# Performance work log

Hardware: AMD Instinct MI355X
Metric: run time of the kernel (lower is better)

## Reference

```python
import jax, jax.numpy as jnp
import numpy as np

NEG = -9e15
ALPHA = 0.2  # leaky relu slope

def setup_inputs() -> dict:
    key = jax.random.key(0)
    k1, k2, k3, k4 = jax.random.split(key, 4)
    N, Fin, Fout = 8192, 512, 256
    h = jax.random.normal(k1, (N, Fin), dtype=jnp.float32)
    adj = jax.random.randint(k2, (N, N), 0, 2, dtype=jnp.int32)
    # xavier_uniform with gain=1.414
    gain = 1.414
    limW = gain * np.sqrt(6.0 / (Fin + Fout))
    W = jax.random.uniform(k3, (Fin, Fout), dtype=jnp.float32, minval=-limW, maxval=limW)
    lima = gain * np.sqrt(6.0 / (2 * Fout + 1))
    a = jax.random.uniform(k4, (2 * Fout, 1), dtype=jnp.float32, minval=-lima, maxval=lima)
    return {"h": h, "adj": adj, "W": W, "a": a}

def reference(h, adj, W, a):
    Fout = W.shape[1]
    Wh = h @ W                                   # [N, Fout]
    # decompose a = [a1; a2]: e_ij = leaky(a1.Wh_i + a2.Wh_j)
    f1 = Wh @ a[:Fout]                           # [N, 1]
    f2 = Wh @ a[Fout:]                           # [N, 1]
    e = jax.nn.leaky_relu(f1 + f2.T, negative_slope=ALPHA)  # [N, N]
    e = jnp.where(adj > 0, e, jnp.float32(NEG))
    attention = jax.nn.softmax(e, axis=1)
    # dropout is identity at inference (training=False)
    h_prime = attention @ Wh                     # [N, Fout]
    return jax.nn.elu(h_prime)
```

## Files before the change

kernel.cpp:

```cpp
#include <hip/hip_runtime.h>
#include <cstdint>
#include <cstddef>

#define ALPHA 0.2f

typedef __attribute__((ext_vector_type(8)))  short short8;
typedef __attribute__((ext_vector_type(16))) float f32x16;

static __device__ __forceinline__ unsigned short f2bf(float x) {
  union { float f; unsigned u; } c; c.f = x;
  unsigned u = c.u;
  unsigned r = (u + 0x7FFFu + ((u >> 16) & 1u)) >> 16;
  return (unsigned short)r;
}
static __device__ __forceinline__ float bf2f(unsigned short b) {
  union { unsigned u; float f; } c; c.u = ((unsigned)b) << 16;
  return c.f;
}

__global__ __launch_bounds__(256, 2) void gemm1(const float* __restrict__ h,
                                                const float* __restrict__ W,
                                                float* __restrict__ Wh) {
  __shared__ float As[32][132];
  __shared__ float Bs[32][64];
  const int t = threadIdx.x;
  const int bid = blockIdx.x;
  const int nb = bid & 3, mb = bid >> 2;
  const int m0 = mb * 128, n0 = nb * 64;
  const int ty = t >> 4, tx = t & 15;
  float acc[8][4];
#pragma unroll
  for (int i = 0; i < 8; i++)
#pragma unroll
    for (int j = 0; j < 4; j++) acc[i][j] = 0.f;

  for (int k0 = 0; k0 < 512; k0 += 32) {
#pragma unroll
    for (int c = 0; c < 4; c++) {
      int m = c * 32 + (t >> 3);
      int kq = (t & 7) * 4;
      float4 v = *(const float4*)&h[(size_t)(m0 + m) * 512 + k0 + kq];
      As[kq + 0][m] = v.x; As[kq + 1][m] = v.y;
      As[kq + 2][m] = v.z; As[kq + 3][m] = v.w;
    }
#pragma unroll
    for (int c = 0; c < 2; c++) {
      int k = c * 16 + (t >> 4);
      int n = (t & 15) * 4;
      *(float4*)&Bs[k][n] = *(const float4*)&W[(size_t)(k0 + k) * 256 + n0 + n];
    }
    __syncthreads();
#pragma unroll
    for (int k = 0; k < 32; k++) {
      float4 a0 = *(float4*)&As[k][ty * 8];
      float4 a1 = *(float4*)&As[k][ty * 8 + 4];
      float4 b  = *(float4*)&Bs[k][tx * 4];
      float av[8] = {a0.x, a0.y, a0.z, a0.w, a1.x, a1.y, a1.z, a1.w};
      float bv[4] = {b.x, b.y, b.z, b.w};
#pragma unroll
      for (int i = 0; i < 8; i++)
#pragma unroll
        for (int j = 0; j < 4; j++) acc[i][j] = fmaf(av[i], bv[j], acc[i][j]);
    }
    __syncthreads();
  }
#pragma unroll
  for (int i = 0; i < 8; i++) {
    float4 v = {acc[i][0], acc[i][1], acc[i][2], acc[i][3]};
    *(float4*)&Wh[(size_t)(m0 + ty * 8 + i) * 256 + n0 + tx * 4] = v;
  }
}

__global__ __launch_bounds__(256) void rowstats(const float* __restrict__ Wh,
                                                const float* __restrict__ a,
                                                float* __restrict__ f1,
                                                float* __restrict__ f2,
                                                unsigned* __restrict__ uvpack,
                                                unsigned short* __restrict__ WhT) {
  const int t = threadIdx.x;
  const int w = t >> 6, lane = t & 63;
  const int i = blockIdx.x * 4 + w;
  float4 wv = *(const float4*)&Wh[(size_t)i * 256 + lane * 4];
  float4 a1 = *(const float4*)&a[lane * 4];
  float4 a2 = *(const float4*)&a[256 + lane * 4];
  float s1 = wv.x * a1.x + wv.y * a1.y + wv.z * a1.z + wv.w * a1.w;
  float s2 = wv.x * a2.x + wv.y * a2.y + wv.z * a2.z + wv.w * a2.w;
#pragma unroll
  for (int off = 32; off; off >>= 1) { s1 += __shfl_xor(s1, off); s2 += __shfl_xor(s2, off); }
  const float wvv[4] = {wv.x, wv.y, wv.z, wv.w};
#pragma unroll
  for (int c = 0; c < 4; c++)
    WhT[(size_t)(lane * 4 + c) * 8192 + i] = f2bf(wvv[c]);
  if (lane == 0) {
    f1[i] = s1; f2[i] = s2;
    float u = __expf(s2), v = __expf(ALPHA * s2);
    uvpack[i] = (unsigned)f2bf(u) | ((unsigned)f2bf(v) << 16);
  }
}

__global__ __launch_bounds__(256) void f2max_k(const float* __restrict__ f2,
                                               float* __restrict__ f2maxp) {
  __shared__ float red[256];
  const int t = threadIdx.x;
  float m = -1e30f;
  for (int c = 0; c < 32; c++) m = fmaxf(m, f2[c * 256 + t]);
  red[t] = m;
  __syncthreads();
  for (int s = 128; s; s >>= 1) {
    if (t < s) red[t] = fmaxf(red[t], red[t + s]);
    __syncthreads();
  }
  if (t == 0) f2maxp[0] = red[0];
}

__global__ __launch_bounds__(256, 2) void attn_main(const int* __restrict__ adj,
                                                    const float* __restrict__ f1,
                                                    const unsigned* __restrict__ uvpack,
                                                    const unsigned short* __restrict__ WhT,
                                                    const float* __restrict__ f2maxp,
                                                    float* __restrict__ accP,
                                                    float* __restrict__ lP) {
  __shared__ unsigned uvs[4096];
  __shared__ __align__(16) unsigned short Pt[32][40];
  __shared__ float lred[32][8];
  const int t = threadIdx.x;
  const int bid = blockIdx.x;
  const int jh = bid & 1;
  const int rb = bid >> 1;
  const int r0 = rb * 32;
  const int jbase = jh * 4096;

#pragma unroll
  for (int c = 0; c < 4; c++) {
    int idx = c * 1024 + t * 4;
    *(uint4*)&uvs[idx] = *(const uint4*)&uvpack[jbase + idx];
  }

  const int r = t >> 3, q = t & 7;
  const float F2max = f2maxp[0];
  const float f1v = f1[r0 + r];
  const float x = f1v + F2max;
  const float M = x > 0.f ? x : ALPHA * x;
  const float Ai = __expf(f1v - M);
  const float Bi = __expf(ALPHA * f1v - M);
  const float Ui = __expf(-f1v);

  const int lane = t & 63, wave = t >> 6;
  const int am = lane & 31, asel = lane >> 5;
  f32x16 acc0 = {}; f32x16 acc1 = {};
  float lpriv = 0.f;

  const int* adjp = adj + (size_t)(r0 + r) * 8192 + jbase + q * 4;
  const unsigned short* bp0 = WhT + (size_t)(wave * 64 + am) * 8192 + jbase + asel * 8;
  const unsigned short* bp1 = bp0 + (size_t)32 * 8192;

  __syncthreads();

  int4 av = *(const int4*)adjp; adjp += 32;
  for (int s = 0; s < 128; s++) {
    int4 avn;
    if (s < 127) { avn = *(const int4*)adjp; }
    adjp += 32;
    uint4 uvq = *(const uint4*)&uvs[s * 32 + q * 4];
    const unsigned uv[4] = {uvq.x, uvq.y, uvq.z, uvq.w};
    const int ad[4] = {av.x, av.y, av.z, av.w};
    float wgt[4];
#pragma unroll
    for (int jj = 0; jj < 4; jj++) {
      float u = bf2f((unsigned short)(uv[jj] & 0xFFFFu));
      float v = bf2f((unsigned short)(uv[jj] >> 16));
      float wv = (u > Ui) ? Ai * u : Bi * v;
      wv = (ad[jj] > 0) ? wv : 0.f;
      wgt[jj] = wv;
    }
    lpriv += (wgt[0] + wgt[1]) + (wgt[2] + wgt[3]);
    unsigned p0 = (unsigned)f2bf(wgt[0]) | ((unsigned)f2bf(wgt[1]) << 16);
    unsigned p1 = (unsigned)f2bf(wgt[2]) | ((unsigned)f2bf(wgt[3]) << 16);
    uint2 pw; pw.x = p0; pw.y = p1;
    *(uint2*)&Pt[r][q * 4] = pw;
    __syncthreads();
#pragma unroll
    for (int hh = 0; hh < 2; hh++) {
      short8 afrag = *(const short8*)&Pt[am][hh * 16 + asel * 8];
      short8 bf0 = *(const short8*)(bp0 + (size_t)s * 32 + hh * 16);
      short8 bf1 = *(const short8*)(bp1 + (size_t)s * 32 + hh * 16);
      acc0 = __builtin_amdgcn_mfma_f32_32x32x16_bf16(afrag, bf0, acc0, 0, 0, 0);
      acc1 = __builtin_amdgcn_mfma_f32_32x32x16_bf16(afrag, bf1, acc1, 0, 0, 0);
    }
    __syncthreads();
    av = avn;
  }

  const size_t base = (size_t)jh * (8192 * 256);
#pragma unroll
  for (int reg = 0; reg < 16; reg++) {
    int rowl = (reg & 3) + 8 * (reg >> 2) + 4 * asel;
    int col = wave * 64 + am;
    accP[base + (size_t)(r0 + rowl) * 256 + col] = acc0[reg];
    accP[base + (size_t)(r0 + rowl) * 256 + col + 32] = acc1[reg];
  }
  lred[r][q] = lpriv;
  __syncthreads();
  if (q == 0) {
    float ssum = 0.f;
#pragma unroll
    for (int k = 0; k < 8; k++) ssum += lred[r][k];
    lP[jh * 8192 + r0 + r] = ssum;
  }
}

__global__ __launch_bounds__(256) void combine(const float* __restrict__ accP,
                                               const float* __restrict__ lP,
                                               float* __restrict__ out) {
  const int idx = (blockIdx.x * 256 + threadIdx.x) * 4;
  const int row = idx >> 8;
  float4 a0 = *(const float4*)&accP[idx];
  float4 a1 = *(const float4*)&accP[(size_t)8192 * 256 + idx];
  float l = lP[row] + lP[8192 + row];
  float inv = 1.0f / fmaxf(l, 1e-30f);
  float vv[4] = {(a0.x + a1.x) * inv, (a0.y + a1.y) * inv,
                 (a0.z + a1.z) * inv, (a0.w + a1.w) * inv};
  float4 o;
  o.x = vv[0] > 0.f ? vv[0] : __expf(vv[0]) - 1.f;
  o.y = vv[1] > 0.f ? vv[1] : __expf(vv[1]) - 1.f;
  o.z = vv[2] > 0.f ? vv[2] : __expf(vv[2]) - 1.f;
  o.w = vv[3] > 0.f ? vv[3] : __expf(vv[3]) - 1.f;
  *(float4*)&out[idx] = o;
}

extern "C" void kernel_launch(void* const* d_in, const int* in_sizes, int n_in,
                              void* d_out, int out_size, void* d_ws, size_t ws_size,
                              hipStream_t stream) {
  const float* h  = (const float*)d_in[0];
  const int* adj  = (const int*)d_in[1];
  const float* W  = (const float*)d_in[2];
  const float* a  = (const float*)d_in[3];
  float* out = (float*)d_out;
  char* ws = (char*)d_ws;

  float* Wh            = (float*)ws;
  float* accP          = (float*)ws;
  unsigned short* WhT  = (unsigned short*)(ws + (size_t)(16u << 20));
  float* f1            = (float*)(ws + (size_t)(20u << 20));
  float* f2            = (float*)(ws + (size_t)(20u << 20) + (32u << 10));
  unsigned* uvpack     = (unsigned*)(ws + (size_t)(20u << 20) + (64u << 10));
  float* f2maxp        = (float*)(ws + (size_t)(20u << 20) + (96u << 10));
  float* lP            = (float*)(ws + (size_t)(20u << 20) + (97u << 10));

  gemm1<<<256, 256, 0, stream>>>(h, W, Wh);
  rowstats<<<2048, 256, 0, stream>>>(Wh, a, f1, f2, uvpack, WhT);
  f2max_k<<<1, 256, 0, stream>>>(f2, f2maxp);
  attn_main<<<512, 256, 0, stream>>>(adj, f1, uvpack, WhT, f2maxp, accP, lP);
  combine<<<2048, 256, 0, stream>>>(accP, lP, out);
}
```

Before: 568.1 us.

## Split-K gemm1, tiled transpose, atomic f2 max, batched double-buffered attention with more splits

The first GEMM is split along K into two partial outputs that later kernels sum, which doubles the block count. The scattered bf16 transpose moves into a separate LDS-tiled kernel, and the single-block f2 max reduction becomes an atomicMax on an order-preserving key. The attention kernel processes four 32-column steps per barrier with a double-buffered, XOR-swizzled P tile and higher occupancy. It uses 4 column splits when the workspace allows, at the cost of extra partial-accumulator traffic in combine.

```diff
diff --git a/kernel.cpp b/kernel.cpp
--- a/kernel.cpp
+++ b/kernel.cpp
@@ -10,8 +10,7 @@
 static __device__ __forceinline__ unsigned short f2bf(float x) {
   union { float f; unsigned u; } c; c.f = x;
   unsigned u = c.u;
-  unsigned r = (u + 0x7FFFu + ((u >> 16) & 1u)) >> 16;
-  return (unsigned short)r;
+  return (unsigned short)((u + 0x7FFFu + ((u >> 16) & 1u)) >> 16);
 }
 static __device__ __forceinline__ float bf2f(unsigned short b) {
   union { unsigned u; float f; } c; c.u = ((unsigned)b) << 16;
@@ -20,13 +19,13 @@
 
 __global__ __launch_bounds__(256, 2) void gemm1(const float* __restrict__ h,
                                                 const float* __restrict__ W,
-                                                float* __restrict__ Wh) {
+                                                float* __restrict__ Whp) {
   __shared__ float As[32][132];
   __shared__ float Bs[32][64];
   const int t = threadIdx.x;
   const int bid = blockIdx.x;
-  const int nb = bid & 3, mb = bid >> 2;
-  const int m0 = mb * 128, n0 = nb * 64;
+  const int nb = bid & 3, kb = (bid >> 2) & 1, mb = bid >> 3;
+  const int m0 = mb * 128, n0 = nb * 64, kbase = kb * 256;
   const int ty = t >> 4, tx = t & 15;
   float acc[8][4];
 #pragma unroll
@@ -34,7 +33,7 @@
 #pragma unroll
     for (int j = 0; j < 4; j++) acc[i][j] = 0.f;
 
-  for (int k0 = 0; k0 < 512; k0 += 32) {
+  for (int k0 = kbase; k0 < kbase + 256; k0 += 32) {
 #pragma unroll
     for (int c = 0; c < 4; c++) {
       int m = c * 32 + (t >> 3);
@@ -64,81 +63,98 @@
     }
     __syncthreads();
   }
+  float* dst = Whp + (size_t)kb * (8192 * 256);
 #pragma unroll
   for (int i = 0; i < 8; i++) {
     float4 v = {acc[i][0], acc[i][1], acc[i][2], acc[i][3]};
-    *(float4*)&Wh[(size_t)(m0 + ty * 8 + i) * 256 + n0 + tx * 4] = v;
-  }
-}
-
-__global__ __launch_bounds__(256) void rowstats(const float* __restrict__ Wh,
+    *(float4*)&dst[(size_t)(m0 + ty * 8 + i) * 256 + n0 + tx * 4] = v;
+  }
+}
+
+__global__ __launch_bounds__(256) void rowstats(const float* __restrict__ Whp,
                                                 const float* __restrict__ a,
                                                 float* __restrict__ f1,
-                                                float* __restrict__ f2,
                                                 unsigned* __restrict__ uvpack,
-                                                unsigned short* __restrict__ WhT) {
+                                                unsigned* __restrict__ f2key) {
   const int t = threadIdx.x;
   const int w = t >> 6, lane = t & 63;
   const int i = blockIdx.x * 4 + w;
-  float4 wv = *(const float4*)&Wh[(size_t)i * 256 + lane * 4];
+  const size_t off = (size_t)i * 256 + lane * 4;
+  float4 v0 = *(const float4*)&Whp[off];
+  float4 v1 = *(const float4*)&Whp[(size_t)8192 * 256 + off];
+  float4 wv = {v0.x + v1.x, v0.y + v1.y, v0.z + v1.z, v0.w + v1.w};
   float4 a1 = *(const float4*)&a[lane * 4];
   float4 a2 = *(const float4*)&a[256 + lane * 4];
   float s1 = wv.x * a1.x + wv.y * a1.y + wv.z * a1.z + wv.w * a1.w;
   float s2 = wv.x * a2.x + wv.y * a2.y + wv.z * a2.z + wv.w * a2.w;
 #pragma unroll
-  for (int off = 32; off; off >>= 1) { s1 += __shfl_xor(s1, off); s2 += __shfl_xor(s2, off); }
-  const float wvv[4] = {wv.x, wv.y, wv.z, wv.w};
-#pragma unroll
-  for (int c = 0; c < 4; c++)
-    WhT[(size_t)(lane * 4 + c) * 8192 + i] = f2bf(wvv[c]);
+  for (int o = 32; o; o >>= 1) { s1 += __shfl_xor(s1, o); s2 += __shfl_xor(s2, o); }
   if (lane == 0) {
-    f1[i] = s1; f2[i] = s2;
+    f1[i] = s1;
     float u = __expf(s2), v = __expf(ALPHA * s2);
     uvpack[i] = (unsigned)f2bf(u) | ((unsigned)f2bf(v) << 16);
-  }
-}
-
-__global__ __launch_bounds__(256) void f2max_k(const float* __restrict__ f2,
-                                               float* __restrict__ f2maxp) {
-  __shared__ float red[256];
-  const int t = threadIdx.x;
-  float m = -1e30f;
-  for (int c = 0; c < 32; c++) m = fmaxf(m, f2[c * 256 + t]);
-  red[t] = m;
+    unsigned ub = __float_as_uint(s2);
+    unsigned key = (ub & 0x80000000u) ? ~ub : (ub | 0x80000000u);
+    atomicMax(f2key, key);
+  }
+}
+
+__global__ __launch_bounds__(256) void transpose_k(const float* __restrict__ Whp,
+                                                   unsigned short* __restrict__ WhT) {
+  __shared__ unsigned short tile[64][264];
+  const int t = threadIdx.x;
+  const int i0 = (blockIdx.x >> 2) * 256, c0 = (blockIdx.x & 3) * 64;
+#pragma unroll
+  for (int it = 0; it < 16; it++) {
+    int i = it * 16 + (t >> 4);
+    int cq = (t & 15) * 4;
+    size_t off = (size_t)(i0 + i) * 256 + c0 + cq;
+    float4 v0 = *(const float4*)&Whp[off];
+    float4 v1 = *(const float4*)&Whp[(size_t)8192 * 256 + off];
+    tile[cq + 0][i] = f2bf(v0.x + v1.x);
+    tile[cq + 1][i] = f2bf(v0.y + v1.y);
+    tile[cq + 2][i] = f2bf(v0.z + v1.z);
+    tile[cq + 3][i] = f2bf(v0.w + v1.w);
+  }
   __syncthreads();
-  for (int s = 128; s; s >>= 1) {
-    if (t < s) red[t] = fmaxf(red[t], red[t + s]);
-    __syncthreads();
-  }
-  if (t == 0) f2maxp[0] = red[0];
-}
-
-__global__ __launch_bounds__(256, 2) void attn_main(const int* __restrict__ adj,
-                                                    const float* __restrict__ f1,
-                                                    const unsigned* __restrict__ uvpack,
-                                                    const unsigned short* __restrict__ WhT,
-                                                    const float* __restrict__ f2maxp,
-                                                    float* __restrict__ accP,
-                                                    float* __restrict__ lP) {
-  __shared__ unsigned uvs[4096];
-  __shared__ __align__(16) unsigned short Pt[32][40];
+  const int c = t >> 2, seg = t & 3;
+#pragma unroll
+  for (int k = 0; k < 8; k++) {
+    int io = (k * 4 + seg) * 8;
+    *(uint4*)&WhT[(size_t)(c0 + c) * 8192 + i0 + io] = *(const uint4*)&tile[c][io];
+  }
+}
+
+template <int JW>
+__global__ __launch_bounds__(256, 4) void attn_main(const int* __restrict__ adj,
+    const float* __restrict__ f1p, const unsigned* __restrict__ uvpack,
+    const unsigned short* __restrict__ WhT, const unsigned* __restrict__ f2key,
+    float* __restrict__ accP, float* __restrict__ lP) {
+  constexpr int JS = 8192 / JW;
+  constexpr int NSTEP = JW / 32;
+  constexpr int KSTEP = 4;
+  constexpr int G = NSTEP / KSTEP;
+  __shared__ unsigned uvs[JW];
+  __shared__ unsigned short Pt[2][32][KSTEP * 32];
   __shared__ float lred[32][8];
   const int t = threadIdx.x;
   const int bid = blockIdx.x;
-  const int jh = bid & 1;
-  const int rb = bid >> 1;
+  const int js = bid & (JS - 1);
+  const int rb = bid / JS;
   const int r0 = rb * 32;
-  const int jbase = jh * 4096;
-
-#pragma unroll
-  for (int c = 0; c < 4; c++) {
+  const int jbase = js * JW;
+
+#pragma unroll
+  for (int c = 0; c < JW / 1024; c++) {
     int idx = c * 1024 + t * 4;
     *(uint4*)&uvs[idx] = *(const uint4*)&uvpack[jbase + idx];
   }
 
   const int r = t >> 3, q = t & 7;
-  const float F2max = f2maxp[0];
-  const float f1v = f1[r0 + r];
+  unsigned key = *f2key;
+  unsigned ub = (key & 0x80000000u) ? (key & 0x7FFFFFFFu) : ~key;
+  const float F2max = __uint_as_float(ub);
+  const float f1v = f1p[r0 + r];
   const float x = f1v + F2max;
   const float M = x > 0.f ? x : ALPHA * x;
   const float Ai = __expf(f1v - M);
@@ -147,79 +163,96 @@
 
   const int lane = t & 63, wave = t >> 6;
   const int am = lane & 31, asel = lane >> 5;
-  f32x16 acc0 = {}; f32x16 acc1 = {};
+  f32x16 acc0 = {}, acc1 = {};
   float lpriv = 0.f;
 
   const int* adjp = adj + (size_t)(r0 + r) * 8192 + jbase + q * 4;
-  const unsigned short* bp0 = WhT + (size_t)(wave * 64 + am) * 8192 + jbase + asel * 8;
-  const unsigned short* bp1 = bp0 + (size_t)32 * 8192;
+  const unsigned short* bp = WhT + (size_t)(wave * 64 + am) * 8192 + jbase + asel * 8;
+
+  int4 av[KSTEP], avn[KSTEP] = {};
+#pragma unroll
+  for (int k = 0; k < KSTEP; k++) av[k] = *(const int4*)(adjp + k * 32);
+  adjp += KSTEP * 32;
 
   __syncthreads();
 
-  int4 av = *(const int4*)adjp; adjp += 32;
-  for (int s = 0; s < 128; s++) {
-    int4 avn;
-    if (s < 127) { avn = *(const int4*)adjp; }
-    adjp += 32;
-    uint4 uvq = *(const uint4*)&uvs[s * 32 + q * 4];
-    const unsigned uv[4] = {uvq.x, uvq.y, uvq.z, uvq.w};
-    const int ad[4] = {av.x, av.y, av.z, av.w};
-    float wgt[4];
-#pragma unroll
-    for (int jj = 0; jj < 4; jj++) {
-      float u = bf2f((unsigned short)(uv[jj] & 0xFFFFu));
-      float v = bf2f((unsigned short)(uv[jj] >> 16));
-      float wv = (u > Ui) ? Ai * u : Bi * v;
-      wv = (ad[jj] > 0) ? wv : 0.f;
-      wgt[jj] = wv;
-    }
-    lpriv += (wgt[0] + wgt[1]) + (wgt[2] + wgt[3]);
-    unsigned p0 = (unsigned)f2bf(wgt[0]) | ((unsigned)f2bf(wgt[1]) << 16);
-    unsigned p1 = (unsigned)f2bf(wgt[2]) | ((unsigned)f2bf(wgt[3]) << 16);
-    uint2 pw; pw.x = p0; pw.y = p1;
-    *(uint2*)&Pt[r][q * 4] = pw;
+  for (int g = 0; g < G; g++) {
+    const int buf = g & 1;
+#pragma unroll
+    for (int k = 0; k < KSTEP; k++) {
+      uint4 uvq = *(const uint4*)&uvs[(g * KSTEP + k) * 32 + q * 4];
+      const unsigned uv[4] = {uvq.x, uvq.y, uvq.z, uvq.w};
+      const int ad[4] = {av[k].x, av[k].y, av[k].z, av[k].w};
+      float wgt[4];
+#pragma unroll
+      for (int jj = 0; jj < 4; jj++) {
+        float u = bf2f((unsigned short)(uv[jj] & 0xFFFFu));
+        float v = bf2f((unsigned short)(uv[jj] >> 16));
+        float wv = (u > Ui) ? Ai * u : Bi * v;
+        wgt[jj] = (ad[jj] > 0) ? wv : 0.f;
+      }
+      lpriv += (wgt[0] + wgt[1]) + (wgt[2] + wgt[3]);
+      unsigned p0 = (unsigned)f2bf(wgt[0]) | ((unsigned)f2bf(wgt[1]) << 16);
+      unsigned p1 = (unsigned)f2bf(wgt[2]) | ((unsigned)f2bf(wgt[3]) << 16);
+      const int chunk = (k * 4 + (q >> 1)) ^ (r & 7);
+      uint2 pw; pw.x = p0; pw.y = p1;
+      *(uint2*)&Pt[buf][r][chunk * 8 + (q & 1) * 4] = pw;
+    }
     __syncthreads();
-#pragma unroll
-    for (int hh = 0; hh < 2; hh++) {
-      short8 afrag = *(const short8*)&Pt[am][hh * 16 + asel * 8];
-      short8 bf0 = *(const short8*)(bp0 + (size_t)s * 32 + hh * 16);
-      short8 bf1 = *(const short8*)(bp1 + (size_t)s * 32 + hh * 16);
-      acc0 = __builtin_amdgcn_mfma_f32_32x32x16_bf16(afrag, bf0, acc0, 0, 0, 0);
-      acc1 = __builtin_amdgcn_mfma_f32_32x32x16_bf16(afrag, bf1, acc1, 0, 0, 0);
-    }
-    __syncthreads();
-    av = avn;
-  }
-
-  const size_t base = (size_t)jh * (8192 * 256);
+    if (g + 1 < G) {
+#pragma unroll
+      for (int k = 0; k < KSTEP; k++) avn[k] = *(const int4*)(adjp + k * 32);
+    }
+    adjp += KSTEP * 32;
+#pragma unroll
+    for (int k = 0; k < KSTEP; k++) {
+#pragma unroll
+      for (int hh = 0; hh < 2; hh++) {
+        const int chunk = (k * 4 + hh * 2 + asel) ^ (am & 7);
+        short8 afrag = *(const short8*)&Pt[buf][am][chunk * 8];
+        const unsigned short* bcol = bp + (size_t)(g * KSTEP + k) * 32 + hh * 16;
+        short8 bf0 = *(const short8*)bcol;
+        short8 bf1 = *(const short8*)(bcol + (size_t)32 * 8192);
+        acc0 = __builtin_amdgcn_mfma_f32_32x32x16_bf16(afrag, bf0, acc0, 0, 0, 0);
+        acc1 = __builtin_amdgcn_mfma_f32_32x32x16_bf16(afrag, bf1, acc1, 0, 0, 0);
+      }
+    }
+#pragma unroll
+    for (int k = 0; k < KSTEP; k++) av[k] = avn[k];
+  }
+
+  const size_t base = (size_t)js * (8192 * 256);
 #pragma unroll
   for (int reg = 0; reg < 16; reg++) {
-    int rowl = (reg & 3) + 8 * (reg >> 2) + 4 * asel;
-    int col = wave * 64 + am;
+    const int rowl = (reg & 3) + 8 * (reg >> 2) + 4 * asel;
+    const int col = wave * 64 + am;
     accP[base + (size_t)(r0 + rowl) * 256 + col] = acc0[reg];
     accP[base + (size_t)(r0 + rowl) * 256 + col + 32] = acc1[reg];
   }
   lred[r][q] = lpriv;
   __syncthreads();
   if (q == 0) {
-    float ssum = 0.f;
-#pragma unroll
-    for (int k = 0; k < 8; k++) ssum += lred[r][k];
-    lP[jh * 8192 + r0 + r] = ssum;
+    float s = 0.f;
+#pragma unroll
+    for (int k = 0; k < 8; k++) s += lred[r][k];
+    lP[(size_t)js * 8192 + r0 + r] = s;
   }
 }
 
 __global__ __launch_bounds__(256) void combine(const float* __restrict__ accP,
                                                const float* __restrict__ lP,
-                                               float* __restrict__ out) {
+                                               float* __restrict__ out, int JS) {
   const int idx = (blockIdx.x * 256 + threadIdx.x) * 4;
   const int row = idx >> 8;
-  float4 a0 = *(const float4*)&accP[idx];
-  float4 a1 = *(const float4*)&accP[(size_t)8192 * 256 + idx];
-  float l = lP[row] + lP[8192 + row];
+  float4 s = {0.f, 0.f, 0.f, 0.f};
+  float l = 0.f;
+  for (int j = 0; j < JS; j++) {
+    float4 a = *(const float4*)&accP[(size_t)j * (8192 * 256) + idx];
+    s.x += a.x; s.y += a.y; s.z += a.z; s.w += a.w;
+    l += lP[(size_t)j * 8192 + row];
+  }
   float inv = 1.0f / fmaxf(l, 1e-30f);
-  float vv[4] = {(a0.x + a1.x) * inv, (a0.y + a1.y) * inv,
-                 (a0.z + a1.z) * inv, (a0.w + a1.w) * inv};
+  float vv[4] = {s.x * inv, s.y * inv, s.z * inv, s.w * inv};
   float4 o;
   o.x = vv[0] > 0.f ? vv[0] : __expf(vv[0]) - 1.f;
   o.y = vv[1] > 0.f ? vv[1] : __expf(vv[1]) - 1.f;
@@ -235,21 +268,28 @@
   const int* adj  = (const int*)d_in[1];
   const float* W  = (const float*)d_in[2];
   const float* a  = (const float*)d_in[3];
-  float* out = (float*)d_out;
   char* ws = (char*)d_ws;
-
-  float* Wh            = (float*)ws;
+  const size_t NF = (size_t)8192 * 256;
+
+  const int JS = (ws_size >= ((size_t)38 << 20)) ? 4 : 2;
+
+  float* Whp           = (float*)ws;
   float* accP          = (float*)ws;
-  unsigned short* WhT  = (unsigned short*)(ws + (size_t)(16u << 20));
-  float* f1            = (float*)(ws + (size_t)(20u << 20));
-  float* f2            = (float*)(ws + (size_t)(20u << 20) + (32u << 10));
-  unsigned* uvpack     = (unsigned*)(ws + (size_t)(20u << 20) + (64u << 10));
-  float* f2maxp        = (float*)(ws + (size_t)(20u << 20) + (96u << 10));
-  float* lP            = (float*)(ws + (size_t)(20u << 20) + (97u << 10));
-
-  gemm1<<<256, 256, 0, stream>>>(h, W, Wh);
-  rowstats<<<2048, 256, 0, stream>>>(Wh, a, f1, f2, uvpack, WhT);
-  f2max_k<<<1, 256, 0, stream>>>(f2, f2maxp);
-  attn_main<<<512, 256, 0, stream>>>(adj, f1, uvpack, WhT, f2maxp, accP, lP);
-  combine<<<2048, 256, 0, stream>>>(accP, lP, out);
-}
+  const size_t accB    = (size_t)JS * NF * 4;
+  unsigned short* WhT  = (unsigned short*)(ws + accB);
+  char* sm             = ws + accB + ((size_t)4 << 20);
+  float* f1            = (float*)sm;
+  unsigned* uvpack     = (unsigned*)(sm + (32 << 10));
+  unsigned* f2key      = (unsigned*)(sm + (64 << 10));
+  float* lP            = (float*)(sm + (65 << 10));
+
+  hipMemsetAsync(f2key, 0, 4, stream);
+  gemm1<<<512, 256, 0, stream>>>(h, W, Whp);
+  transpose_k<<<128, 256, 0, stream>>>(Whp, WhT);
+  rowstats<<<2048, 256, 0, stream>>>(Whp, a, f1, uvpack, f2key);
+  if (JS == 4)
+    attn_main<2048><<<1024, 256, 0, stream>>>(adj, f1, uvpack, WhT, f2key, accP, lP);
+  else
+    attn_main<4096><<<512, 256, 0, stream>>>(adj, f1, uvpack, WhT, f2key, accP, lP);
+  combine<<<2048, 256, 0, stream>>>(accP, lP, (float*)d_out, JS);
+}
```

Result: slower. 624.7 us (+10.0%).
